# Kernel tuning notes

Measured on AMD Instinct MI355X. Metric: run time of the kernel, lower is better.

## Reference

```python
import jax, jax.numpy as jnp
import numpy as np

CHAMFER_W, NORMAL_W, EDGE_W, WATERTIGHT_W, SDF_W = 1.0, 0.5, 0.3, 0.2, 1.0
DIHEDRAL_THRESHOLD = 0.5
EPS_COS = 1e-8   # F.cosine_similarity eps
EPS_NRM = 1e-12  # F.normalize eps


def _pairwise_sqdist(p, g):
    # (B,N,3),(B,M,3) -> (B,N,M) squared distances, without (B,N,M,3) temp
    p2 = (p * p).sum(-1)
    g2 = (g * g).sum(-1)
    return p2[:, :, None] + g2[:, None, :] - 2.0 * jnp.einsum('bnd,bmd->bnm', p, g)


def _face_normals(verts, faces):
    v0, v1, v2 = verts[faces[:, 0]], verts[faces[:, 1]], verts[faces[:, 2]]
    n = jnp.cross(v1 - v0, v2 - v0)
    return n / jnp.maximum(jnp.linalg.norm(n, axis=-1, keepdims=True), EPS_NRM)


def _edge_structure(faces, num_verts):
    # All 3F directed edges (f_i, f_{(i+1)%3}), canonicalized to sorted keys.
    a = faces                      # (F,3)
    b = jnp.roll(faces, -1, axis=1)  # pairs (0,1),(1,2),(2,0)
    lo = jnp.minimum(a, b).reshape(-1)
    hi = jnp.maximum(a, b).reshape(-1)
    keys = lo * num_verts + hi      # unique int key per undirected edge (< 2^31)
    face_ids = jnp.repeat(jnp.arange(faces.shape[0], dtype=jnp.int32), 3)
    order = jnp.argsort(keys, stable=True)
    sk = keys[order]
    sf = face_ids[order]
    E = sk.shape[0]
    run_start = jnp.concatenate([jnp.array([True]), sk[1:] != sk[:-1]])
    eq_next = jnp.concatenate([sk[:-1] == sk[1:], jnp.array([False])])
    rs_pad = jnp.concatenate([run_start, jnp.array([True, True])])
    # pair2[i]: run of length exactly 2 starting at i -> faces sf[i], sf[i+1]
    pair2 = run_start & eq_next & rs_pad[2:]
    return sf, pair2, run_start


def _edge_sharpness(verts, faces):
    normals = _face_normals(verts, faces)
    sf, pair2, _ = _edge_structure(faces, verts.shape[0])
    sf_next = jnp.roll(sf, -1)
    cos = (normals[sf] * normals[sf_next]).sum(-1)
    terms = jax.nn.relu(cos - DIHEDRAL_THRESHOLD)
    cnt = pair2.sum()
    return jnp.where(cnt > 0, (terms * pair2).sum() / jnp.maximum(cnt, 1), 0.0)


def _watertight(faces, num_verts):
    _, pair2, run_start = _edge_structure(faces, num_verts)
    total = run_start.sum()
    bad = total - pair2.sum()
    return jnp.where(total > 0, bad.astype(jnp.float32) / jnp.maximum(total, 1).astype(jnp.float32), 0.0)


def setup_inputs():
    key = jax.random.key(0)
    ks = jax.random.split(key, 10)
    B, N, M, V, F, NS = 1, 8192, 8192, 20000, 40000, 65536
    return {
        'pred_sdf': jax.random.normal(ks[0], (B, NS, 1), jnp.float32),
        'gt_sdf': jax.random.normal(ks[1], (B, NS, 1), jnp.float32),
        'extracted_vertices': jax.random.normal(ks[2], (V, 3), jnp.float32),
        'extracted_faces': jax.random.randint(ks[3], (F, 3), 0, V, jnp.int32),
        'gt_vertices': jax.random.normal(ks[4], (V, 3), jnp.float32),
        'gt_faces': jax.random.randint(ks[5], (F, 3), 0, V, jnp.int32),
        'pred_points': jax.random.normal(ks[6], (B, N, 3), jnp.float32),
        'gt_points': jax.random.normal(ks[7], (B, M, 3), jnp.float32),
        'pred_normals': jax.random.normal(ks[8], (B, N, 3), jnp.float32),
        'gt_normals': jax.random.normal(ks[9], (B, M, 3), jnp.float32),
    }


def reference(pred_sdf, gt_sdf, extracted_vertices, extracted_faces, gt_vertices, gt_faces,
              pred_points, gt_points, pred_normals, gt_normals):
    # sdf supervision (L1)
    sdf_l = SDF_W * jnp.abs(pred_sdf - gt_sdf).mean()

    # chamfer
    dist = _pairwise_sqdist(pred_points, gt_points)  # (B,N,M)
    min_p2g = dist.min(axis=2).mean(axis=1)
    min_g2p = dist.min(axis=1).mean(axis=1)
    chamfer_l = CHAMFER_W * (min_p2g + min_g2p).mean()

    # normal consistency (nearest GT point per pred point)
    nn_idx = jnp.argmin(dist, axis=2)  # (B,N)
    matched = jnp.take_along_axis(gt_normals, nn_idx[..., None], axis=1)  # (B,N,3)
    pn = jnp.maximum(jnp.linalg.norm(pred_normals, axis=-1), EPS_COS)
    gn = jnp.maximum(jnp.linalg.norm(matched, axis=-1), EPS_COS)
    cos = (pred_normals * matched).sum(-1) / (pn * gn)
    normal_l = NORMAL_W * (1.0 - jnp.abs(cos)).mean()

    # edge sharpness (GT mesh args are unused by the original implementation)
    edge_l = EDGE_W * _edge_sharpness(extracted_vertices, extracted_faces)

    # watertight regularization
    wt_l = WATERTIGHT_W * _watertight(extracted_faces, extracted_vertices.shape[0])

    total = sdf_l + chamfer_l + normal_l + edge_l + wt_l
    return sdf_l, chamfer_l, normal_l, edge_l, wt_l, total
```

## Files before the change

kernel.cpp:

```cpp
#include <hip/hip_runtime.h>
#include <math.h>

#define TILE 128
#define REG 8
#define APB (256 * REG)
#define HASH_C 262144
#define HASH_MASK (HASH_C - 1)
#define EMPTY_SLOT 0xFFFFFFFFu
#define KEY_MASK ((1u << 29) - 1)
#define CNT_ONE (1u << 29)

#define SBIAS 256.0f
#define TOPBITS 0x42000000u
#define PADW 480.0f


__device__ inline float waveReduceF(float v) {
#pragma unroll
  for (int off = 32; off > 0; off >>= 1) v += __shfl_down(v, off, 64);
  return v;
}

__global__ __launch_bounds__(256) void fused_kernel(
    const float* __restrict__ P, const float* __restrict__ G, int N, int M,
    int meshBlocks, int p2gBlocks, int nTileG, int nTileP,
    unsigned long long* __restrict__ p2g, unsigned* __restrict__ g2p,
    const float* __restrict__ verts, const int* __restrict__ faces, int F, int V,
    float4* __restrict__ fn, unsigned* __restrict__ slots,
    unsigned* __restrict__ face0, unsigned* __restrict__ face1,
    unsigned* __restrict__ cnt, unsigned* __restrict__ pairList,
    float* accumF, unsigned* accumU) {
  __shared__ float4 tile[TILE];
  int tid = threadIdx.x;

  if (blockIdx.x == 0 && tid == 0) {
#pragma unroll
    for (int q = 0; q < 5; q++) accumF[q] = 0.f;
    accumU[0] = 0u;
  }

  if ((int)blockIdx.x < meshBlocks) {
    int e = blockIdx.x * 256 + tid;
    bool valid = (e < 3 * F);
    unsigned c = 0xFFu;
    if (valid) {
      int f = e / 3, k = e - 3 * f;
      int a = faces[3 * f + k];
      int b = faces[3 * f + ((k + 1) % 3)];
      if (k == 0) {
        int i1 = faces[3 * f + 1], i2 = faces[3 * f + 2];
        float ax = verts[3 * a], ay = verts[3 * a + 1], az = verts[3 * a + 2];
        float bx = verts[3 * i1] - ax, by = verts[3 * i1 + 1] - ay, bz = verts[3 * i1 + 2] - az;
        float cx = verts[3 * i2] - ax, cy = verts[3 * i2 + 1] - ay, cz = verts[3 * i2 + 2] - az;
        float nx = by * cz - bz * cy;
        float ny = bz * cx - bx * cz;
        float nz = bx * cy - by * cx;
        float l = sqrtf(nx * nx + ny * ny + nz * nz);
        float inv = 1.f / fmaxf(l, 1e-12f);
        fn[f] = make_float4(nx * inv, ny * inv, nz * inv, 0.f);
      }
      unsigned lo = (unsigned)min(a, b), hi = (unsigned)max(a, b);
      unsigned key = lo * (unsigned)V + hi + 1u;
      unsigned h = (key * 2654435761u) & HASH_MASK;
      for (;;) {
        unsigned prev = atomicCAS(&slots[h], EMPTY_SLOT, key | CNT_ONE);
        if (prev == EMPTY_SLOT) { c = 0u; break; }
        if ((prev & KEY_MASK) == key) {
          c = (atomicAdd(&slots[h], CNT_ONE) >> 29) & 7u;
          break;
        }
        h = (h + 1) & HASH_MASK;
      }
      if (c == 0u) face0[h] = (unsigned)f;
      else if (c == 1u) {
        face1[h] = (unsigned)f;
        unsigned idx = atomicAdd(&cnt[2], 1u) + 1u;
        pairList[idx] = h;
      }
    }
    unsigned long long b0 = __ballot(valid && c == 0u);
    unsigned long long b1 = __ballot(valid && c == 1u);
    unsigned long long b2 = __ballot(valid && c == 2u);
    if ((tid & 63) == 0) {
      unsigned d = (unsigned)__popcll(b0);
      unsigned pd = (unsigned)__popcll(b1) - (unsigned)__popcll(b2);
      if (d) atomicAdd(&cnt[0], d);
      if (pd) atomicAdd(&cnt[1], pd);
    }
    return;
  }

  int bid = blockIdx.x - meshBlocks;
  bool isP2G = (bid < p2gBlocks);
  const float* A;
  const float* B;
  int nA, nB, chunk, tileIdx;
  if (isP2G) {
    chunk = bid / nTileG;
    tileIdx = bid % nTileG;
    A = P; nA = N; B = G; nB = M;
  } else {
    int b2 = bid - p2gBlocks;
    chunk = b2 / nTileP;
    tileIdx = b2 % nTileP;
    A = G; nA = M; B = P; nB = N;
  }

  int abase = chunk * APB + tid;
  float px[REG], py[REG], pz[REG];
#pragma unroll
  for (int r = 0; r < REG; r++) {
    int i = abase + 256 * r;
    if (i < nA) { px[r] = A[3 * i]; py[r] = A[3 * i + 1]; pz[r] = A[3 * i + 2]; }
    else        { px[r] = 0.f; py[r] = 0.f; pz[r] = 0.f; }
  }

  int tbase = tileIdx * TILE;
  if (tid < TILE) {
    int j = tbase + tid;
    float4 v;
    if (j < nB) {
      float x = B[3 * j], y = B[3 * j + 1], z = B[3 * j + 2];
      v = make_float4(x, y, z, fmaf(0.5f, x * x + y * y + z * z, SBIAS));
    } else {
      v = make_float4(0.f, 0.f, 0.f, PADW);
    }
    tile[tid] = v;
  }
  __syncthreads();

  if (isP2G) {
    unsigned best[REG];
#pragma unroll
    for (int r = 0; r < REG; r++) best[r] = 0xFFFFFFFFu;
#pragma unroll 2
    for (int j = 0; j < TILE; j += 4) {
      float4 g0 = tile[j];
      float4 g1 = tile[j + 1];
      float4 g2 = tile[j + 2];
      float4 g3 = tile[j + 3];
#pragma unroll
      for (int r = 0; r < REG; r++) {
        float s0 = fmaf(-pz[r], g0.z, fmaf(-py[r], g0.y, fmaf(-px[r], g0.x, g0.w)));
        float s1 = fmaf(-pz[r], g1.z, fmaf(-py[r], g1.y, fmaf(-px[r], g1.x, g1.w)));
        float s2 = fmaf(-pz[r], g2.z, fmaf(-py[r], g2.y, fmaf(-px[r], g2.x, g2.w)));
        float s3 = fmaf(-pz[r], g3.z, fmaf(-py[r], g3.y, fmaf(-px[r], g3.x, g3.w)));
        unsigned k0 = (__float_as_uint(s0) << 7) | (unsigned)j;
        unsigned k1 = (__float_as_uint(s1) << 7) | (unsigned)(j + 1);
        unsigned k2 = (__float_as_uint(s2) << 7) | (unsigned)(j + 2);
        unsigned k3 = (__float_as_uint(s3) << 7) | (unsigned)(j + 3);
        best[r] = min(min(best[r], min(k0, k1)), min(k2, k3));
      }
    }
#pragma unroll
    for (int r = 0; r < REG; r++) {
      int i = abase + 256 * r;
      if (i < nA) {
        unsigned sbits = (best[r] >> 7) | TOPBITS;
        unsigned idx = (unsigned)tbase + (best[r] & 127u);
        unsigned long long packed = ((unsigned long long)sbits << 32) | idx;
        atomicMin(&p2g[i], packed);
      }
    }
  } else {
    float best[REG];
#pragma unroll
    for (int r = 0; r < REG; r++) best[r] = INFINITY;
#pragma unroll 2
    for (int j = 0; j < TILE; j += 4) {
      float4 g0 = tile[j];
      float4 g1 = tile[j + 1];
      float4 g2 = tile[j + 2];
      float4 g3 = tile[j + 3];
#pragma unroll
      for (int r = 0; r < REG; r++) {
        float s0 = fmaf(-pz[r], g0.z, fmaf(-py[r], g0.y, fmaf(-px[r], g0.x, g0.w)));
        float s1 = fmaf(-pz[r], g1.z, fmaf(-py[r], g1.y, fmaf(-px[r], g1.x, g1.w)));
        float s2 = fmaf(-pz[r], g2.z, fmaf(-py[r], g2.y, fmaf(-px[r], g2.x, g2.w)));
        float s3 = fmaf(-pz[r], g3.z, fmaf(-py[r], g3.y, fmaf(-px[r], g3.x, g3.w)));
        best[r] = fminf(fminf(best[r], fminf(s0, s1)), fminf(s2, s3));
      }
    }
#pragma unroll
    for (int r = 0; r < REG; r++) {
      int i = abase + 256 * r;
      if (i < nA) atomicMin(&g2p[i], __float_as_uint(best[r]));
    }
  }
}

__global__ __launch_bounds__(256) void finalize_kernel(
    const float* __restrict__ P, const float* __restrict__ G,
    const float* __restrict__ PN, const float* __restrict__ GN,
    const float* __restrict__ sdfA, const float* __restrict__ sdfB,
    const unsigned* __restrict__ slots, const unsigned* __restrict__ face0,
    const unsigned* __restrict__ face1, const float4* __restrict__ fn,
    const unsigned* __restrict__ cnt, const unsigned* __restrict__ pairList,
    int N, int M, int NS, int nBlocks,
    const unsigned long long* __restrict__ p2g, const unsigned* __restrict__ g2p,
    float* accumF, unsigned* accumU, float* out) {
  __shared__ float sh[20];
  int t = blockIdx.x * 256 + threadIdx.x;
  int stride = nBlocks * 256;
  float sp = 0.f, sg = 0.f, sn = 0.f, ss = 0.f, term = 0.f;
  if (t < N) {
    unsigned long long pk = p2g[t];
    float sprime = __uint_as_float((unsigned)(pk >> 32));
    int idx = (int)(pk & 0xFFFFFFFFull);
    float px = P[3 * t], py = P[3 * t + 1], pz = P[3 * t + 2];
    sp = px * px + py * py + pz * pz + 2.f * sprime - 2.f * SBIAS;
    float nx = PN[3 * t], ny = PN[3 * t + 1], nz = PN[3 * t + 2];
    float mx = GN[3 * idx], my = GN[3 * idx + 1], mz = GN[3 * idx + 2];
    float pn = fmaxf(sqrtf(nx * nx + ny * ny + nz * nz), 1e-8f);
    float gn = fmaxf(sqrtf(mx * mx + my * my + mz * mz), 1e-8f);
    float cosv = (nx * mx + ny * my + nz * mz) / (pn * gn);
    sn = 1.f - fabsf(cosv);
  }
  if (t < M) {
    float sprime = __uint_as_float(g2p[t]);
    float gx = G[3 * t], gy = G[3 * t + 1], gz = G[3 * t + 2];
    sg = gx * gx + gy * gy + gz * gz + 2.f * sprime - 2.f * SBIAS;
  }
  for (int i = t; i < NS; i += stride) ss += fabsf(sdfA[i] - sdfB[i]);
  unsigned listLen = cnt[2] + 1u;
  for (unsigned i = (unsigned)t; i < listLen; i += (unsigned)stride) {
    unsigned h = pairList[i];
    if ((slots[h] >> 29) == 2u) {
      float4 n0 = fn[face0[h]];
      float4 n1 = fn[face1[h]];
      float c = n0.x * n1.x + n0.y * n1.y + n0.z * n1.z;
      term += fmaxf(c - 0.5f, 0.f);
    }
  }
  sp = waveReduceF(sp);
  sg = waveReduceF(sg);
  sn = waveReduceF(sn);
  ss = waveReduceF(ss);
  term = waveReduceF(term);
  int lane = threadIdx.x & 63, wid = threadIdx.x >> 6;
  if (lane == 0) {
    sh[wid] = sp; sh[4 + wid] = sg; sh[8 + wid] = sn; sh[12 + wid] = ss;
    sh[16 + wid] = term;
  }
  __syncthreads();
  if (threadIdx.x == 0) {
    atomicAdd(&accumF[1], sh[0] + sh[1] + sh[2] + sh[3]);
    atomicAdd(&accumF[2], sh[4] + sh[5] + sh[6] + sh[7]);
    atomicAdd(&accumF[3], sh[8] + sh[9] + sh[10] + sh[11]);
    atomicAdd(&accumF[0], sh[12] + sh[13] + sh[14] + sh[15]);
    atomicAdd(&accumF[4], sh[16] + sh[17] + sh[18] + sh[19]);
    __threadfence();
    unsigned ticket = atomicAdd(&accumU[0], 1u);
    if (ticket == (unsigned)(nBlocks - 1)) {
      float a0 = atomicAdd(&accumF[0], 0.f);
      float a1 = atomicAdd(&accumF[1], 0.f);
      float a2 = atomicAdd(&accumF[2], 0.f);
      float a3 = atomicAdd(&accumF[3], 0.f);
      float a4 = atomicAdd(&accumF[4], 0.f);
      float runsF = (float)(cnt[0] + 1u);
      float pairsF = (float)(cnt[1] + 1u);
      float sdf = a0 / (float)NS;
      float chamfer = a1 / (float)N + a2 / (float)M;
      float normal = 0.5f * (a3 / (float)N);
      float edge = (pairsF > 0.f) ? 0.3f * (a4 / pairsF) : 0.f;
      float wt = (runsF > 0.f) ? 0.2f * ((runsF - pairsF) / runsF) : 0.f;
      out[0] = sdf;
      out[1] = chamfer;
      out[2] = normal;
      out[3] = edge;
      out[4] = wt;
      out[5] = sdf + chamfer + normal + edge + wt;
    }
  }
}

extern "C" void kernel_launch(void* const* d_in, const int* in_sizes, int n_in,
                              void* d_out, int out_size, void* d_ws,
                              size_t ws_size, hipStream_t stream) {
  const float* pred_sdf = (const float*)d_in[0];
  const float* gt_sdf   = (const float*)d_in[1];
  const float* ev       = (const float*)d_in[2];
  const int*   ef       = (const int*)d_in[3];
  const float* pp       = (const float*)d_in[6];
  const float* gp       = (const float*)d_in[7];
  const float* pn       = (const float*)d_in[8];
  const float* gn       = (const float*)d_in[9];
  int NS = in_sizes[0];
  int V = in_sizes[2] / 3;
  int F = in_sizes[3] / 3;
  int N = in_sizes[6] / 3;
  int M = in_sizes[7] / 3;
  float* out = (float*)d_out;

  char* ws = (char*)d_ws;
  size_t offSlots = 0;
  size_t offP2G = offSlots + (size_t)HASH_C * 4;
  size_t offG2P = offP2G + (size_t)N * 8;
  size_t offCnt = offG2P + (size_t)M * 4;
  size_t ffBytes = offCnt + 16;
  size_t offAccumF = (ffBytes + 63) & ~(size_t)63;
  size_t offAccumU = offAccumF + 32;
  size_t offFace0 = offAccumU + 32;
  size_t offFace1 = offFace0 + (size_t)HASH_C * 4;
  size_t offFN = (offFace1 + (size_t)HASH_C * 4 + 15) & ~(size_t)15;
  size_t offPairList = offFN + (size_t)F * 16;

  unsigned* slots = (unsigned*)(ws + offSlots);
  unsigned long long* p2gArr = (unsigned long long*)(ws + offP2G);
  unsigned* g2pArr = (unsigned*)(ws + offG2P);
  unsigned* cnt = (unsigned*)(ws + offCnt);
  float* accumF = (float*)(ws + offAccumF);
  unsigned* accumU = (unsigned*)(ws + offAccumU);
  unsigned* face0 = (unsigned*)(ws + offFace0);
  unsigned* face1 = (unsigned*)(ws + offFace1);
  float4* fnorm = (float4*)(ws + offFN);
  unsigned* pairList = (unsigned*)(ws + offPairList);

  hipMemsetAsync(ws, 0xFF, ffBytes, stream);

  int nChunkP = (N + APB - 1) / APB, nTileG = (M + TILE - 1) / TILE;
  int nChunkG = (M + APB - 1) / APB, nTileP = (N + TILE - 1) / TILE;
  int p2gBlocks = nChunkP * nTileG;
  int chamferBlocks = p2gBlocks + nChunkG * nTileP;
  int meshBlocks = (3 * F + 255) / 256;
  fused_kernel<<<meshBlocks + chamferBlocks, 256, 0, stream>>>(
      pp, gp, N, M, meshBlocks, p2gBlocks, nTileG, nTileP, p2gArr, g2pArr,
      ev, ef, F, V, fnorm, slots, face0, face1, cnt, pairList, accumF, accumU);

  int mx = (N > M ? N : M);
  int nFin = (mx + 255) / 256;
  if (nFin < 64) nFin = 64;
  finalize_kernel<<<nFin, 256, 0, stream>>>(
      pp, gp, pn, gn, pred_sdf, gt_sdf, slots, face0, face1, fnorm,
      cnt, pairList, N, M, NS, nFin, p2gArr, g2pArr, accumF, accumU, out);
}
```

Measured before the change: 120.4 us.

## Move SDF L1 reduction into fused kernel and reorder block roles

The SDF absolute-difference reduction moves out of the finalize kernel into 32 extra blocks of the fused kernel, which write per-block partial sums that finalize then adds up. Block order changes so chamfer blocks come first, then the mesh hashing blocks, then the SDF blocks. The chamfer inner loop drops from four to two candidate points per iteration, which cuts register pressure but adds loop overhead. The intent is to overlap the SDF reduction with the chamfer work and shorten the finalize kernel's tail.

```diff
diff --git a/kernel.cpp b/kernel.cpp
--- a/kernel.cpp
+++ b/kernel.cpp
@@ -9,6 +9,7 @@
 #define EMPTY_SLOT 0xFFFFFFFFu
 #define KEY_MASK ((1u << 29) - 1)
 #define CNT_ONE (1u << 29)
+#define SDF_BLOCKS 32
 
 #define SBIAS 256.0f
 #define TOPBITS 0x42000000u
@@ -23,14 +24,16 @@
 
 __global__ __launch_bounds__(256) void fused_kernel(
     const float* __restrict__ P, const float* __restrict__ G, int N, int M,
-    int meshBlocks, int p2gBlocks, int nTileG, int nTileP,
+    int p2gBlocks, int chamferBlocks, int meshBlocks, int nTileG, int nTileP,
     unsigned long long* __restrict__ p2g, unsigned* __restrict__ g2p,
     const float* __restrict__ verts, const int* __restrict__ faces, int F, int V,
     float4* __restrict__ fn, unsigned* __restrict__ slots,
     unsigned* __restrict__ face0, unsigned* __restrict__ face1,
     unsigned* __restrict__ cnt, unsigned* __restrict__ pairList,
-    float* accumF, unsigned* accumU) {
+    const float* __restrict__ sdfA, const float* __restrict__ sdfB, int NS,
+    float* __restrict__ sdfPartial, float* accumF, unsigned* accumU) {
   __shared__ float4 tile[TILE];
+  __shared__ float shS[4];
   int tid = threadIdx.x;
 
   if (blockIdx.x == 0 && tid == 0) {
@@ -39,8 +42,22 @@
     accumU[0] = 0u;
   }
 
-  if ((int)blockIdx.x < meshBlocks) {
-    int e = blockIdx.x * 256 + tid;
+  if ((int)blockIdx.x >= chamferBlocks + meshBlocks) {
+    int sb = blockIdx.x - chamferBlocks - meshBlocks;
+    int t = sb * 256 + tid;
+    int strideS = SDF_BLOCKS * 256;
+    float ss = 0.f;
+    for (int i = t; i < NS; i += strideS) ss += fabsf(sdfA[i] - sdfB[i]);
+    ss = waveReduceF(ss);
+    int lane = tid & 63, wid = tid >> 6;
+    if (lane == 0) shS[wid] = ss;
+    __syncthreads();
+    if (tid == 0) sdfPartial[sb] = shS[0] + shS[1] + shS[2] + shS[3];
+    return;
+  }
+
+  if ((int)blockIdx.x >= chamferBlocks) {
+    int e = (blockIdx.x - chamferBlocks) * 256 + tid;
     bool valid = (e < 3 * F);
     unsigned c = 0xFFu;
     if (valid) {
@@ -90,19 +107,18 @@
     return;
   }
 
-  int bid = blockIdx.x - meshBlocks;
-  bool isP2G = (bid < p2gBlocks);
+  bool isP2G = ((int)blockIdx.x < p2gBlocks);
   const float* A;
   const float* B;
   int nA, nB, chunk, tileIdx;
   if (isP2G) {
-    chunk = bid / nTileG;
-    tileIdx = bid % nTileG;
+    chunk = blockIdx.x / nTileG;
+    tileIdx = blockIdx.x % nTileG;
     A = P; nA = N; B = G; nB = M;
   } else {
-    int b2 = bid - p2gBlocks;
-    chunk = b2 / nTileP;
-    tileIdx = b2 % nTileP;
+    int bid = blockIdx.x - p2gBlocks;
+    chunk = bid / nTileP;
+    tileIdx = bid % nTileP;
     A = G; nA = M; B = P; nB = N;
   }
 
@@ -134,22 +150,16 @@
 #pragma unroll
     for (int r = 0; r < REG; r++) best[r] = 0xFFFFFFFFu;
 #pragma unroll 2
-    for (int j = 0; j < TILE; j += 4) {
+    for (int j = 0; j < TILE; j += 2) {
       float4 g0 = tile[j];
       float4 g1 = tile[j + 1];
-      float4 g2 = tile[j + 2];
-      float4 g3 = tile[j + 3];
 #pragma unroll
       for (int r = 0; r < REG; r++) {
         float s0 = fmaf(-pz[r], g0.z, fmaf(-py[r], g0.y, fmaf(-px[r], g0.x, g0.w)));
         float s1 = fmaf(-pz[r], g1.z, fmaf(-py[r], g1.y, fmaf(-px[r], g1.x, g1.w)));
-        float s2 = fmaf(-pz[r], g2.z, fmaf(-py[r], g2.y, fmaf(-px[r], g2.x, g2.w)));
-        float s3 = fmaf(-pz[r], g3.z, fmaf(-py[r], g3.y, fmaf(-px[r], g3.x, g3.w)));
         unsigned k0 = (__float_as_uint(s0) << 7) | (unsigned)j;
         unsigned k1 = (__float_as_uint(s1) << 7) | (unsigned)(j + 1);
-        unsigned k2 = (__float_as_uint(s2) << 7) | (unsigned)(j + 2);
-        unsigned k3 = (__float_as_uint(s3) << 7) | (unsigned)(j + 3);
-        best[r] = min(min(best[r], min(k0, k1)), min(k2, k3));
+        best[r] = min(best[r], min(k0, k1));
       }
     }
 #pragma unroll
@@ -167,18 +177,14 @@
 #pragma unroll
     for (int r = 0; r < REG; r++) best[r] = INFINITY;
 #pragma unroll 2
-    for (int j = 0; j < TILE; j += 4) {
+    for (int j = 0; j < TILE; j += 2) {
       float4 g0 = tile[j];
       float4 g1 = tile[j + 1];
-      float4 g2 = tile[j + 2];
-      float4 g3 = tile[j + 3];
 #pragma unroll
       for (int r = 0; r < REG; r++) {
         float s0 = fmaf(-pz[r], g0.z, fmaf(-py[r], g0.y, fmaf(-px[r], g0.x, g0.w)));
         float s1 = fmaf(-pz[r], g1.z, fmaf(-py[r], g1.y, fmaf(-px[r], g1.x, g1.w)));
-        float s2 = fmaf(-pz[r], g2.z, fmaf(-py[r], g2.y, fmaf(-px[r], g2.x, g2.w)));
-        float s3 = fmaf(-pz[r], g3.z, fmaf(-py[r], g3.y, fmaf(-px[r], g3.x, g3.w)));
-        best[r] = fminf(fminf(best[r], fminf(s0, s1)), fminf(s2, s3));
+        best[r] = fminf(best[r], fminf(s0, s1));
       }
     }
 #pragma unroll
@@ -192,7 +198,7 @@
 __global__ __launch_bounds__(256) void finalize_kernel(
     const float* __restrict__ P, const float* __restrict__ G,
     const float* __restrict__ PN, const float* __restrict__ GN,
-    const float* __restrict__ sdfA, const float* __restrict__ sdfB,
+    const float* __restrict__ sdfPartial,
     const unsigned* __restrict__ slots, const unsigned* __restrict__ face0,
     const unsigned* __restrict__ face1, const float4* __restrict__ fn,
     const unsigned* __restrict__ cnt, const unsigned* __restrict__ pairList,
@@ -221,7 +227,7 @@
     float gx = G[3 * t], gy = G[3 * t + 1], gz = G[3 * t + 2];
     sg = gx * gx + gy * gy + gz * gz + 2.f * sprime - 2.f * SBIAS;
   }
-  for (int i = t; i < NS; i += stride) ss += fabsf(sdfA[i] - sdfB[i]);
+  if (t < SDF_BLOCKS) ss = sdfPartial[t];
   unsigned listLen = cnt[2] + 1u;
   for (unsigned i = (unsigned)t; i < listLen; i += (unsigned)stride) {
     unsigned h = pairList[i];
@@ -304,6 +310,7 @@
   size_t offFace1 = offFace0 + (size_t)HASH_C * 4;
   size_t offFN = (offFace1 + (size_t)HASH_C * 4 + 15) & ~(size_t)15;
   size_t offPairList = offFN + (size_t)F * 16;
+  size_t offSdfP = offPairList + (size_t)(3 * F) * 4;
 
   unsigned* slots = (unsigned*)(ws + offSlots);
   unsigned long long* p2gArr = (unsigned long long*)(ws + offP2G);
@@ -315,6 +322,7 @@
   unsigned* face1 = (unsigned*)(ws + offFace1);
   float4* fnorm = (float4*)(ws + offFN);
   unsigned* pairList = (unsigned*)(ws + offPairList);
+  float* sdfPartial = (float*)(ws + offSdfP);
 
   hipMemsetAsync(ws, 0xFF, ffBytes, stream);
 
@@ -323,14 +331,15 @@
   int p2gBlocks = nChunkP * nTileG;
   int chamferBlocks = p2gBlocks + nChunkG * nTileP;
   int meshBlocks = (3 * F + 255) / 256;
-  fused_kernel<<<meshBlocks + chamferBlocks, 256, 0, stream>>>(
-      pp, gp, N, M, meshBlocks, p2gBlocks, nTileG, nTileP, p2gArr, g2pArr,
-      ev, ef, F, V, fnorm, slots, face0, face1, cnt, pairList, accumF, accumU);
+  fused_kernel<<<chamferBlocks + meshBlocks + SDF_BLOCKS, 256, 0, stream>>>(
+      pp, gp, N, M, p2gBlocks, chamferBlocks, meshBlocks, nTileG, nTileP,
+      p2gArr, g2pArr, ev, ef, F, V, fnorm, slots, face0, face1, cnt, pairList,
+      pred_sdf, gt_sdf, NS, sdfPartial, accumF, accumU);
 
   int mx = (N > M ? N : M);
   int nFin = (mx + 255) / 256;
   if (nFin < 64) nFin = 64;
   finalize_kernel<<<nFin, 256, 0, stream>>>(
-      pp, gp, pn, gn, pred_sdf, gt_sdf, slots, face0, face1, fnorm,
+      pp, gp, pn, gn, sdfPartial, slots, face0, face1, fnorm,
       cnt, pairList, N, M, NS, nFin, p2gArr, g2pArr, accumF, accumU, out);
 }
```

Result: faster. 117.0 us (median of 2 runs) (-2.8%).
